# Kernel optimization log

Measured on AMD Instinct MI355X. Metric: run time of the kernel, lower is better.

## Reference

```python
import jax, jax.numpy as jnp
import numpy as np


def adder2d(x, w, stride=1, padding=0):
    """AdderNet conv: out = -sum_{ci,kh,kw} |x_patch - w|, supports groups.
    x: [B,Cin,H,W], w: [Cout, Cin//G, K, K]. Loops only over K*K kernel taps."""
    B, Cin, H, W = x.shape
    Cout, Cin_g, K, _ = w.shape
    G = Cin // Cin_g
    Co_g = Cout // G
    xp = jnp.pad(x, ((0, 0), (0, 0), (padding, padding), (padding, padding)))
    Ho = (H + 2 * padding - K) // stride + 1
    Wo = (W + 2 * padding - K) // stride + 1
    wg = w.reshape(G, Co_g, Cin_g, K, K)
    out = jnp.zeros((B, Cout, Ho, Wo), x.dtype)
    for kh in range(K):
        for kw in range(K):
            xs = jax.lax.slice(
                xp, (0, 0, kh, kw),
                (B, Cin, kh + stride * (Ho - 1) + 1, kw + stride * (Wo - 1) + 1),
                (1, 1, stride, stride))  # [B,Cin,Ho,Wo]
            xs = xs.reshape(B, G, 1, Cin_g, Ho, Wo)
            wt = wg[:, :, :, kh, kw][None, :, :, :, None, None]  # [1,G,Co_g,Cin_g,1,1]
            out = out - jnp.abs(xs - wt).sum(3).reshape(B, Cout, Ho, Wo)
    return out


def bn(x, g, b, m, v, eps=1e-5):
    inv = g / jnp.sqrt(v + eps)
    return x * inv[None, :, None, None] + (b - m * inv)[None, :, None, None]


def setup_inputs() -> dict:
    key = jax.random.key(0)
    ks = jax.random.split(key, 18)
    d = {}
    d["x"] = jax.random.normal(ks[0], (8, 256, 28, 28), jnp.float32)
    d["w1"] = jax.random.normal(ks[1], (64, 256, 1, 1), jnp.float32) * 0.05
    d["w_peg"] = jax.random.normal(ks[2], (64, 1, 3, 3), jnp.float32) * 0.05
    d["w2"] = jax.random.normal(ks[3], (64, 64, 3, 3), jnp.float32) * 0.05
    d["w3"] = jax.random.normal(ks[4], (256, 64, 1, 1), jnp.float32) * 0.05
    for i, (c, tag) in enumerate([(64, "1"), (64, "2"), (256, "3")]):
        d["g" + tag] = jax.random.uniform(ks[5 + 4 * i], (c,), jnp.float32, 0.5, 1.5)
        d["b" + tag] = jax.random.normal(ks[6 + 4 * i], (c,), jnp.float32) * 0.1
        d["m" + tag] = jax.random.normal(ks[7 + 4 * i], (c,), jnp.float32) * 0.1
        d["v" + tag] = jax.random.uniform(ks[8 + 4 * i], (c,), jnp.float32, 0.5, 1.5)
    return d


def reference(x, w1, w_peg, w2, w3, g1, b1, m1, v1, g2, b2, m2, v2, g3, b3, m3, v3):
    residual = x  # downsample is Identity (stride=1, inplanes==outplanes)
    h = adder2d(x, w1)                       # 1x1 adder conv 256->64
    h = adder2d(h, w_peg, stride=1, padding=1)  # PEG: depthwise 3x3 adder conv
    h = jax.nn.relu(bn(h, g1, b1, m1, v1))
    h = adder2d(h, w2, padding=1)            # 3x3 adder conv 64->64
    h = jax.nn.relu(bn(h, g2, b2, m2, v2))
    h = adder2d(h, w3)                       # 1x1 adder conv 64->256
    h = bn(h, g3, b3, m3, v3)
    return jax.nn.relu(h + residual)
```

## Files before the change

### kernel.cpp

```cpp
#include <hip/hip_runtime.h>
#include <math.h>

#define HW 28
#define PR 30
#define PC 32
#define PPAD (PR * PC)

__device__ __forceinline__ void tap3(const float4 a, const float2 b,
                                     const float w0, const float w1, const float w2,
                                     float4& acc) {
    acc.x += fabsf(a.x - w0) + fabsf(a.y - w1) + fabsf(a.z - w2);
    acc.y += fabsf(a.y - w0) + fabsf(a.z - w1) + fabsf(a.w - w2);
    acc.z += fabsf(a.z - w0) + fabsf(a.w - w1) + fabsf(b.x - w2);
    acc.w += fabsf(a.w - w0) + fabsf(b.x - w1) + fabsf(b.y - w2);
}

__global__ __launch_bounds__(448) void k1_adder1x1(const float* __restrict__ x,
                                                   const float* __restrict__ w1,
                                                   float* __restrict__ h1p) {
    __shared__ float  ws[256 * 20];
    __shared__ float4 pl[1792];
    const int tid    = threadIdx.x;
    const int cog    = tid & 3;
    const int pxg    = (tid >> 2) % 14;
    const int cic    = tid / 56;
    const int n      = blockIdx.x / 14;
    const int p0     = (blockIdx.x % 14) * 56 + pxg * 4;
    const int cobase = blockIdx.y * 16;

    for (int idx = tid; idx < 16 * 256; idx += 448) {
        int co = idx >> 8, ci = idx & 255;
        ws[ci * 20 + co] = w1[(size_t)(cobase + co) * 256 + ci];
    }
    __syncthreads();

    float4 acc0 = {0,0,0,0}, acc1 = acc0, acc2 = acc0, acc3 = acc0;
    const float* xp = x + ((size_t)n * 256 + cic * 32) * 784 + p0;
    const float* wp = ws + cic * 32 * 20 + cog * 4;
    #pragma unroll 4
    for (int i = 0; i < 32; ++i) {
        float4 u = *(const float4*)(xp + (size_t)i * 784);
        float4 w = *(const float4*)(wp + i * 20);
        acc0.x += fabsf(u.x - w.x); acc0.y += fabsf(u.y - w.x); acc0.z += fabsf(u.z - w.x); acc0.w += fabsf(u.w - w.x);
        acc1.x += fabsf(u.x - w.y); acc1.y += fabsf(u.y - w.y); acc1.z += fabsf(u.z - w.y); acc1.w += fabsf(u.w - w.y);
        acc2.x += fabsf(u.x - w.z); acc2.y += fabsf(u.y - w.z); acc2.z += fabsf(u.z - w.z); acc2.w += fabsf(u.w - w.z);
        acc3.x += fabsf(u.x - w.w); acc3.y += fabsf(u.y - w.w); acc3.z += fabsf(u.z - w.w); acc3.w += fabsf(u.w - w.w);
    }
    const int pbase = pxg * 16 + cog * 4;
    pl[cic * 224 + pbase + 0] = acc0;
    pl[cic * 224 + pbase + 1] = acc1;
    pl[cic * 224 + pbase + 2] = acc2;
    pl[cic * 224 + pbase + 3] = acc3;
    __syncthreads();

    if (tid < 224) {
        const int j = cic;
        float4 s = pl[pbase + j];
        #pragma unroll
        for (int c = 1; c < 8; ++c) {
            float4 t = pl[c * 224 + pbase + j];
            s.x += t.x; s.y += t.y; s.z += t.z; s.w += t.w;
        }
        const int co = cobase + cog * 4 + j;
        const int y = p0 / 28, xx = p0 % 28;
        float* op = h1p + ((size_t)(n * 64 + co) * PR + y + 1) * PC + xx + 1;
        op[0] = -s.x; op[1] = -s.y; op[2] = -s.z; op[3] = -s.w;
    }
}

__global__ __launch_bounds__(256) void k2_peg_bn_relu(const float* __restrict__ h1p,
                                                      const float* __restrict__ wp,
                                                      const float* __restrict__ g1,
                                                      const float* __restrict__ b1,
                                                      const float* __restrict__ m1,
                                                      const float* __restrict__ v1,
                                                      float* __restrict__ h2p) {
    const int t   = blockIdx.x * 256 + threadIdx.x;
    const int pxq = t % 196;
    const int c   = (t / 196) & 63;
    const int n   = t / (196 * 64);
    const int p0  = pxq * 4;
    const int y   = p0 / 28, xx = p0 % 28;

    const float* base = h1p + ((size_t)(n * 64 + c) * PR + y) * PC + xx;
    const float* wc   = wp + c * 9;
    float4 acc = {0,0,0,0};
    #pragma unroll
    for (int kh = 0; kh < 3; ++kh) {
        float4 a = *(const float4*)(base + kh * PC);
        float2 b = *(const float2*)(base + kh * PC + 4);
        tap3(a, b, wc[kh * 3 + 0], wc[kh * 3 + 1], wc[kh * 3 + 2], acc);
    }
    float inv = g1[c] * rsqrtf(v1[c] + 1e-5f);
    float bb  = b1[c] - m1[c] * inv;
    float* op = h2p + ((size_t)(n * 64 + c) * PR + y + 1) * PC + xx + 1;
    op[0] = fmaxf(-acc.x * inv + bb, 0.f);
    op[1] = fmaxf(-acc.y * inv + bb, 0.f);
    op[2] = fmaxf(-acc.z * inv + bb, 0.f);
    op[3] = fmaxf(-acc.w * inv + bb, 0.f);
}

__global__ __launch_bounds__(448) void k3_adder3x3_bn_relu(const float* __restrict__ h2p,
                                                           const float* __restrict__ w2,
                                                           const float* __restrict__ g2,
                                                           const float* __restrict__ b2,
                                                           const float* __restrict__ m2,
                                                           const float* __restrict__ v2,
                                                           float* __restrict__ h3) {
    __shared__ float  ws[576 * 20];
    __shared__ float4 pl[1792];
    const int tid    = threadIdx.x;
    const int cog    = tid & 3;
    const int pxg    = (tid >> 2) % 14;
    const int cic    = tid / 56;
    const int y0     = blockIdx.x * 2;
    const int cobase = blockIdx.y * 16;
    const int n      = blockIdx.z;
    const int yl     = pxg / 7;
    const int xx0    = (pxg % 7) * 4;
    const int Y      = y0 + yl;

    for (int idx = tid; idx < 9216; idx += 448) {
        int co = idx / 576;
        int rem = idx - co * 576;
        ws[rem * 20 + co] = w2[(size_t)(cobase + co) * 576 + rem];
    }
    __syncthreads();

    float4 acc0 = {0,0,0,0}, acc1 = acc0, acc2 = acc0, acc3 = acc0;
    #pragma unroll 2
    for (int i = 0; i < 8; ++i) {
        const float* rp = h2p + ((size_t)(n * 64 + cic * 8 + i) * PR + Y) * PC + xx0;
        const float* wb = ws + (cic * 8 + i) * 180 + cog * 4;
        #pragma unroll
        for (int kh = 0; kh < 3; ++kh) {
            float4 a = *(const float4*)(rp + kh * PC);
            float2 b = *(const float2*)(rp + kh * PC + 4);
            const float* wk = wb + kh * 60;
            float4 w0 = *(const float4*)(wk);
            float4 w1v = *(const float4*)(wk + 20);
            float4 w2v = *(const float4*)(wk + 40);
            tap3(a, b, w0.x, w1v.x, w2v.x, acc0);
            tap3(a, b, w0.y, w1v.y, w2v.y, acc1);
            tap3(a, b, w0.z, w1v.z, w2v.z, acc2);
            tap3(a, b, w0.w, w1v.w, w2v.w, acc3);
        }
    }
    const int pbase = pxg * 16 + cog * 4;
    pl[cic * 224 + pbase + 0] = acc0;
    pl[cic * 224 + pbase + 1] = acc1;
    pl[cic * 224 + pbase + 2] = acc2;
    pl[cic * 224 + pbase + 3] = acc3;
    __syncthreads();

    if (tid < 224) {
        const int j = cic;
        float4 s = pl[pbase + j];
        #pragma unroll
        for (int c = 1; c < 8; ++c) {
            float4 t = pl[c * 224 + pbase + j];
            s.x += t.x; s.y += t.y; s.z += t.z; s.w += t.w;
        }
        const int co = cobase + cog * 4 + j;
        float inv = g2[co] * rsqrtf(v2[co] + 1e-5f);
        float bb  = b2[co] - m2[co] * inv;
        float4 o;
        o.x = fmaxf(-s.x * inv + bb, 0.f);
        o.y = fmaxf(-s.y * inv + bb, 0.f);
        o.z = fmaxf(-s.z * inv + bb, 0.f);
        o.w = fmaxf(-s.w * inv + bb, 0.f);
        *(float4*)(h3 + (size_t)(n * 64 + co) * 784 + Y * 28 + xx0) = o;
    }
}

__global__ __launch_bounds__(448) void k6_adder1x1_bn_res_relu(const float* __restrict__ h3,
                                                               const float* __restrict__ w3,
                                                               const float* __restrict__ x,
                                                               const float* __restrict__ g3,
                                                               const float* __restrict__ b3,
                                                               const float* __restrict__ m3,
                                                               const float* __restrict__ v3,
                                                               float* __restrict__ out) {
    __shared__ float  ws[64 * 36];
    __shared__ float4 pl[1792];
    const int tid    = threadIdx.x;
    const int cog    = tid & 7;
    const int pxg    = (tid >> 3) % 14;
    const int cic    = tid / 112;
    const int n      = blockIdx.x / 14;
    const int p0     = (blockIdx.x % 14) * 56 + pxg * 4;
    const int cobase = blockIdx.y * 32;

    for (int idx = tid; idx < 2048; idx += 448) {
        int co = idx >> 6, ci = idx & 63;
        ws[ci * 36 + co] = w3[(size_t)(cobase + co) * 64 + ci];
    }
    __syncthreads();

    float4 acc0 = {0,0,0,0}, acc1 = acc0, acc2 = acc0, acc3 = acc0;
    const float* hp = h3 + ((size_t)n * 64 + cic * 16) * 784 + p0;
    const float* wp = ws + cic * 16 * 36 + cog * 4;
    #pragma unroll 4
    for (int i = 0; i < 16; ++i) {
        float4 u = *(const float4*)(hp + (size_t)i * 784);
        float4 w = *(const float4*)(wp + i * 36);
        acc0.x += fabsf(u.x - w.x); acc0.y += fabsf(u.y - w.x); acc0.z += fabsf(u.z - w.x); acc0.w += fabsf(u.w - w.x);
        acc1.x += fabsf(u.x - w.y); acc1.y += fabsf(u.y - w.y); acc1.z += fabsf(u.z - w.y); acc1.w += fabsf(u.w - w.y);
        acc2.x += fabsf(u.x - w.z); acc2.y += fabsf(u.y - w.z); acc2.z += fabsf(u.z - w.z); acc2.w += fabsf(u.w - w.z);
        acc3.x += fabsf(u.x - w.w); acc3.y += fabsf(u.y - w.w); acc3.z += fabsf(u.z - w.w); acc3.w += fabsf(u.w - w.w);
    }
    const int pbase = pxg * 32 + cog * 4;
    pl[cic * 448 + pbase + 0] = acc0;
    pl[cic * 448 + pbase + 1] = acc1;
    pl[cic * 448 + pbase + 2] = acc2;
    pl[cic * 448 + pbase + 3] = acc3;
    __syncthreads();

    {
        const int j = cic;
        float4 s = pl[pbase + j];
        #pragma unroll
        for (int c = 1; c < 4; ++c) {
            float4 t = pl[c * 448 + pbase + j];
            s.x += t.x; s.y += t.y; s.z += t.z; s.w += t.w;
        }
        const int co = cobase + cog * 4 + j;
        float inv = g3[co] * rsqrtf(v3[co] + 1e-5f);
        float bb  = b3[co] - m3[co] * inv;
        size_t obase = ((size_t)n * 256 + co) * 784 + p0;
        float4 r = *(const float4*)(x + obase);
        float4 o;
        o.x = fmaxf(-s.x * inv + bb + r.x, 0.f);
        o.y = fmaxf(-s.y * inv + bb + r.y, 0.f);
        o.z = fmaxf(-s.z * inv + bb + r.z, 0.f);
        o.w = fmaxf(-s.w * inv + bb + r.w, 0.f);
        *(float4*)(out + obase) = o;
    }
}

extern "C" void kernel_launch(void* const* d_in, const int* in_sizes, int n_in,
                              void* d_out, int out_size, void* d_ws, size_t ws_size,
                              hipStream_t stream) {
    const float* x  = (const float*)d_in[0];
    const float* w1 = (const float*)d_in[1];
    const float* wp = (const float*)d_in[2];
    const float* w2 = (const float*)d_in[3];
    const float* w3 = (const float*)d_in[4];
    const float* g1 = (const float*)d_in[5];
    const float* b1 = (const float*)d_in[6];
    const float* m1 = (const float*)d_in[7];
    const float* v1 = (const float*)d_in[8];
    const float* g2 = (const float*)d_in[9];
    const float* b2 = (const float*)d_in[10];
    const float* m2 = (const float*)d_in[11];
    const float* v2 = (const float*)d_in[12];
    const float* g3 = (const float*)d_in[13];
    const float* b3 = (const float*)d_in[14];
    const float* m3 = (const float*)d_in[15];
    const float* v3 = (const float*)d_in[16];
    float* out = (float*)d_out;

    float* h1p = (float*)d_ws;
    float* h2p = h1p + 491520;
    float* h3  = h2p + 491520;

    hipMemsetAsync(d_ws, 0, 2u * 491520u * 4u, stream);

    k1_adder1x1<<<dim3(112, 4), 448, 0, stream>>>(x, w1, h1p);
    k2_peg_bn_relu<<<dim3(392), 256, 0, stream>>>(h1p, wp, g1, b1, m1, v1, h2p);
    k3_adder3x3_bn_relu<<<dim3(14, 4, 8), 448, 0, stream>>>(h2p, w2, g2, b2, m2, v2, h3);
    k6_adder1x1_bn_res_relu<<<dim3(112, 8), 448, 0, stream>>>(h3, w3, x, g3, b3, m3, v3, out);
}
```

Measured before the change: 67.86 us.

## Fuse four adder-conv stages into two kernels with smem intermediates

Merges the 1x1 adder conv with the depthwise PEG conv and BN1, computing halo rows into shared memory per block. Merges the 3x3 adder conv, BN2, the final 1x1 adder conv, BN3 and the residual into one kernel per output row and image, keeping h3 in shared memory. Drops the h1 and h3 global buffers and the memset by writing the padding borders explicitly. In exchange it gives small grids (256 and 224 blocks), reloads the full w2/w3 weights per block, and recomputes halo rows in the first kernel.

```diff
diff --git a/kernel.cpp b/kernel.cpp
--- a/kernel.cpp
+++ b/kernel.cpp
@@ -1,10 +1,8 @@
 #include <hip/hip_runtime.h>
 #include <math.h>
 
-#define HW 28
 #define PR 30
 #define PC 32
-#define PPAD (PR * PC)
 
 __device__ __forceinline__ void tap3(const float4 a, const float2 b,
                                      const float w0, const float w1, const float w2,
@@ -15,226 +13,211 @@
     acc.w += fabsf(a.w - w0) + fabsf(b.x - w1) + fabsf(b.y - w2);
 }
 
-__global__ __launch_bounds__(448) void k1_adder1x1(const float* __restrict__ x,
-                                                   const float* __restrict__ w1,
-                                                   float* __restrict__ h1p) {
-    __shared__ float  ws[256 * 20];
-    __shared__ float4 pl[1792];
+__global__ __launch_bounds__(448) void ka_fused(const float* __restrict__ x,
+                                                const float* __restrict__ w1,
+                                                const float* __restrict__ wpeg,
+                                                const float* __restrict__ g1,
+                                                const float* __restrict__ b1,
+                                                const float* __restrict__ m1,
+                                                const float* __restrict__ v1,
+                                                float* __restrict__ h2p) {
+    __shared__ __align__(16) float smem[3072];
+    float* wsA = smem;
+    float* h1t = smem + 1024;
     const int tid    = threadIdx.x;
-    const int cog    = tid & 3;
-    const int pxg    = (tid >> 2) % 14;
-    const int cic    = tid / 56;
-    const int n      = blockIdx.x / 14;
-    const int p0     = (blockIdx.x % 14) * 56 + pxg * 4;
-    const int cobase = blockIdx.y * 16;
-
-    for (int idx = tid; idx < 16 * 256; idx += 448) {
-        int co = idx >> 8, ci = idx & 255;
-        ws[ci * 20 + co] = w1[(size_t)(cobase + co) * 256 + ci];
+    const int cobase = blockIdx.x * 4;
+    const int yh     = blockIdx.y;
+    const int n      = blockIdx.z;
+    const int co     = tid / 112;
+    const int rem    = tid % 112;
+    const int row    = rem / 7;
+    const int q      = rem % 7;
+
+    for (int idx = tid; idx < 1024; idx += 448) {
+        int c2 = idx >> 8, ci = idx & 255;
+        wsA[ci * 4 + c2] = w1[(size_t)(cobase + c2) * 256 + ci];
+    }
+    for (int idx = tid; idx < 512; idx += 448)
+        ((float4*)h1t)[idx] = make_float4(0.f, 0.f, 0.f, 0.f);
+    __syncthreads();
+
+    const int gy = yh * 14 - 1 + row;
+    if (gy >= 0 && gy < 28) {
+        float4 acc = {0.f, 0.f, 0.f, 0.f};
+        const float* xp = x + (size_t)n * 256 * 784 + gy * 28 + q * 4;
+        #pragma unroll 8
+        for (int ci = 0; ci < 256; ++ci) {
+            float4 u = *(const float4*)(xp + (size_t)ci * 784);
+            float w  = wsA[ci * 4 + co];
+            acc.x += fabsf(u.x - w); acc.y += fabsf(u.y - w);
+            acc.z += fabsf(u.z - w); acc.w += fabsf(u.w - w);
+        }
+        float* hd = h1t + co * 512 + row * 32 + 1 + q * 4;
+        hd[0] = -acc.x; hd[1] = -acc.y; hd[2] = -acc.z; hd[3] = -acc.w;
+    }
+    __syncthreads();
+
+    if (row < 14) {
+        const int c  = cobase + co;
+        const int oy = yh * 14 + row;
+        const float* wc = wpeg + c * 9;
+        const float* hb = h1t + co * 512 + row * 32 + q * 4;
+        float4 acc = {0.f, 0.f, 0.f, 0.f};
+        #pragma unroll
+        for (int kh = 0; kh < 3; ++kh) {
+            float4 a  = *(const float4*)(hb + kh * 32);
+            float2 bv = *(const float2*)(hb + kh * 32 + 4);
+            tap3(a, bv, wc[kh * 3 + 0], wc[kh * 3 + 1], wc[kh * 3 + 2], acc);
+        }
+        float inv = g1[c] * rsqrtf(v1[c] + 1e-5f);
+        float bb  = b1[c] - m1[c] * inv;
+        float* op = h2p + ((size_t)(n * 64 + c) * PR + oy + 1) * PC + 1 + q * 4;
+        op[0] = fmaxf(-acc.x * inv + bb, 0.f);
+        op[1] = fmaxf(-acc.y * inv + bb, 0.f);
+        op[2] = fmaxf(-acc.z * inv + bb, 0.f);
+        op[3] = fmaxf(-acc.w * inv + bb, 0.f);
+    }
+    for (int idx = tid; idx < 352; idx += 448) {
+        if (idx < 224) {
+            int rr = idx >> 4, k = idx & 15;
+            int cc = k >> 2, kk = k & 3;
+            int col = kk ? 28 + kk : 0;
+            h2p[((size_t)(n * 64 + cobase + cc) * PR + yh * 14 + 1 + rr) * PC + col] = 0.f;
+        } else {
+            int j = idx - 224;
+            int cc = j >> 5, col = j & 31;
+            int prow = yh ? 29 : 0;
+            h2p[((size_t)(n * 64 + cobase + cc) * PR + prow) * PC + col] = 0.f;
+        }
+    }
+}
+
+__global__ __launch_bounds__(448) void kb_fused(const float* __restrict__ h2p,
+                                                const float* __restrict__ w2,
+                                                const float* __restrict__ w3,
+                                                const float* __restrict__ x,
+                                                const float* __restrict__ g2,
+                                                const float* __restrict__ b2,
+                                                const float* __restrict__ m2,
+                                                const float* __restrict__ v2,
+                                                const float* __restrict__ g3,
+                                                const float* __restrict__ b3,
+                                                const float* __restrict__ m3,
+                                                const float* __restrict__ v3,
+                                                float* __restrict__ out) {
+    __shared__ __align__(16) float smem[18688];
+    float*  h3t = smem;
+    float*  h2t = smem + 2048;
+    float*  wck = smem + 8192;
+    float4* pl4 = (float4*)(smem + 2048);
+    float*  w3t = smem + 2048;
+    const int tid    = threadIdx.x;
+    const int Y      = blockIdx.x;
+    const int n      = blockIdx.y;
+    const int cic    = tid / 112;
+    const int rem    = tid % 112;
+    const int colane = rem / 7;
+    const int q      = rem % 7;
+
+    for (int idx = tid; idx < 1536; idx += 448) {
+        int ci = idx / 24, r2 = idx % 24;
+        int r = r2 / 8, c4 = r2 % 8;
+        *(float4*)(h2t + ci * 96 + r * 32 + c4 * 4) =
+            *(const float4*)(h2p + ((size_t)(n * 64 + ci) * PR + Y + r) * PC + c4 * 4);
     }
     __syncthreads();
 
     float4 acc0 = {0,0,0,0}, acc1 = acc0, acc2 = acc0, acc3 = acc0;
-    const float* xp = x + ((size_t)n * 256 + cic * 32) * 784 + p0;
-    const float* wp = ws + cic * 32 * 20 + cog * 4;
-    #pragma unroll 4
-    for (int i = 0; i < 32; ++i) {
-        float4 u = *(const float4*)(xp + (size_t)i * 784);
-        float4 w = *(const float4*)(wp + i * 20);
-        acc0.x += fabsf(u.x - w.x); acc0.y += fabsf(u.y - w.x); acc0.z += fabsf(u.z - w.x); acc0.w += fabsf(u.w - w.x);
-        acc1.x += fabsf(u.x - w.y); acc1.y += fabsf(u.y - w.y); acc1.z += fabsf(u.z - w.y); acc1.w += fabsf(u.w - w.y);
-        acc2.x += fabsf(u.x - w.z); acc2.y += fabsf(u.y - w.z); acc2.z += fabsf(u.z - w.z); acc2.w += fabsf(u.w - w.z);
-        acc3.x += fabsf(u.x - w.w); acc3.y += fabsf(u.y - w.w); acc3.z += fabsf(u.z - w.w); acc3.w += fabsf(u.w - w.w);
-    }
-    const int pbase = pxg * 16 + cog * 4;
-    pl[cic * 224 + pbase + 0] = acc0;
-    pl[cic * 224 + pbase + 1] = acc1;
-    pl[cic * 224 + pbase + 2] = acc2;
-    pl[cic * 224 + pbase + 3] = acc3;
-    __syncthreads();
-
-    if (tid < 224) {
-        const int j = cic;
-        float4 s = pl[pbase + j];
-        #pragma unroll
-        for (int c = 1; c < 8; ++c) {
-            float4 t = pl[c * 224 + pbase + j];
-            s.x += t.x; s.y += t.y; s.z += t.z; s.w += t.w;
-        }
-        const int co = cobase + cog * 4 + j;
-        const int y = p0 / 28, xx = p0 % 28;
-        float* op = h1p + ((size_t)(n * 64 + co) * PR + y + 1) * PC + xx + 1;
-        op[0] = -s.x; op[1] = -s.y; op[2] = -s.z; op[3] = -s.w;
-    }
-}
-
-__global__ __launch_bounds__(256) void k2_peg_bn_relu(const float* __restrict__ h1p,
-                                                      const float* __restrict__ wp,
-                                                      const float* __restrict__ g1,
-                                                      const float* __restrict__ b1,
-                                                      const float* __restrict__ m1,
-                                                      const float* __restrict__ v1,
-                                                      float* __restrict__ h2p) {
-    const int t   = blockIdx.x * 256 + threadIdx.x;
-    const int pxq = t % 196;
-    const int c   = (t / 196) & 63;
-    const int n   = t / (196 * 64);
-    const int p0  = pxq * 4;
-    const int y   = p0 / 28, xx = p0 % 28;
-
-    const float* base = h1p + ((size_t)(n * 64 + c) * PR + y) * PC + xx;
-    const float* wc   = wp + c * 9;
-    float4 acc = {0,0,0,0};
-    #pragma unroll
-    for (int kh = 0; kh < 3; ++kh) {
-        float4 a = *(const float4*)(base + kh * PC);
-        float2 b = *(const float2*)(base + kh * PC + 4);
-        tap3(a, b, wc[kh * 3 + 0], wc[kh * 3 + 1], wc[kh * 3 + 2], acc);
-    }
-    float inv = g1[c] * rsqrtf(v1[c] + 1e-5f);
-    float bb  = b1[c] - m1[c] * inv;
-    float* op = h2p + ((size_t)(n * 64 + c) * PR + y + 1) * PC + xx + 1;
-    op[0] = fmaxf(-acc.x * inv + bb, 0.f);
-    op[1] = fmaxf(-acc.y * inv + bb, 0.f);
-    op[2] = fmaxf(-acc.z * inv + bb, 0.f);
-    op[3] = fmaxf(-acc.w * inv + bb, 0.f);
-}
-
-__global__ __launch_bounds__(448) void k3_adder3x3_bn_relu(const float* __restrict__ h2p,
-                                                           const float* __restrict__ w2,
-                                                           const float* __restrict__ g2,
-                                                           const float* __restrict__ b2,
-                                                           const float* __restrict__ m2,
-                                                           const float* __restrict__ v2,
-                                                           float* __restrict__ h3) {
-    __shared__ float  ws[576 * 20];
-    __shared__ float4 pl[1792];
-    const int tid    = threadIdx.x;
-    const int cog    = tid & 3;
-    const int pxg    = (tid >> 2) % 14;
-    const int cic    = tid / 56;
-    const int y0     = blockIdx.x * 2;
-    const int cobase = blockIdx.y * 16;
-    const int n      = blockIdx.z;
-    const int yl     = pxg / 7;
-    const int xx0    = (pxg % 7) * 4;
-    const int Y      = y0 + yl;
-
-    for (int idx = tid; idx < 9216; idx += 448) {
-        int co = idx / 576;
-        int rem = idx - co * 576;
-        ws[rem * 20 + co] = w2[(size_t)(cobase + co) * 576 + rem];
-    }
-    __syncthreads();
-
-    float4 acc0 = {0,0,0,0}, acc1 = acc0, acc2 = acc0, acc3 = acc0;
-    #pragma unroll 2
-    for (int i = 0; i < 8; ++i) {
-        const float* rp = h2p + ((size_t)(n * 64 + cic * 8 + i) * PR + Y) * PC + xx0;
-        const float* wb = ws + (cic * 8 + i) * 180 + cog * 4;
-        #pragma unroll
-        for (int kh = 0; kh < 3; ++kh) {
-            float4 a = *(const float4*)(rp + kh * PC);
-            float2 b = *(const float2*)(rp + kh * PC + 4);
-            const float* wk = wb + kh * 60;
-            float4 w0 = *(const float4*)(wk);
-            float4 w1v = *(const float4*)(wk + 20);
-            float4 w2v = *(const float4*)(wk + 40);
-            tap3(a, b, w0.x, w1v.x, w2v.x, acc0);
-            tap3(a, b, w0.y, w1v.y, w2v.y, acc1);
-            tap3(a, b, w0.z, w1v.z, w2v.z, acc2);
-            tap3(a, b, w0.w, w1v.w, w2v.w, acc3);
-        }
-    }
-    const int pbase = pxg * 16 + cog * 4;
-    pl[cic * 224 + pbase + 0] = acc0;
-    pl[cic * 224 + pbase + 1] = acc1;
-    pl[cic * 224 + pbase + 2] = acc2;
-    pl[cic * 224 + pbase + 3] = acc3;
-    __syncthreads();
-
-    if (tid < 224) {
-        const int j = cic;
-        float4 s = pl[pbase + j];
-        #pragma unroll
-        for (int c = 1; c < 8; ++c) {
-            float4 t = pl[c * 224 + pbase + j];
-            s.x += t.x; s.y += t.y; s.z += t.z; s.w += t.w;
-        }
-        const int co = cobase + cog * 4 + j;
-        float inv = g2[co] * rsqrtf(v2[co] + 1e-5f);
-        float bb  = b2[co] - m2[co] * inv;
-        float4 o;
-        o.x = fmaxf(-s.x * inv + bb, 0.f);
-        o.y = fmaxf(-s.y * inv + bb, 0.f);
-        o.z = fmaxf(-s.z * inv + bb, 0.f);
-        o.w = fmaxf(-s.w * inv + bb, 0.f);
-        *(float4*)(h3 + (size_t)(n * 64 + co) * 784 + Y * 28 + xx0) = o;
-    }
-}
-
-__global__ __launch_bounds__(448) void k6_adder1x1_bn_res_relu(const float* __restrict__ h3,
-                                                               const float* __restrict__ w3,
-                                                               const float* __restrict__ x,
-                                                               const float* __restrict__ g3,
-                                                               const float* __restrict__ b3,
-                                                               const float* __restrict__ m3,
-                                                               const float* __restrict__ v3,
-                                                               float* __restrict__ out) {
-    __shared__ float  ws[64 * 36];
-    __shared__ float4 pl[1792];
-    const int tid    = threadIdx.x;
-    const int cog    = tid & 7;
-    const int pxg    = (tid >> 3) % 14;
-    const int cic    = tid / 112;
-    const int n      = blockIdx.x / 14;
-    const int p0     = (blockIdx.x % 14) * 56 + pxg * 4;
-    const int cobase = blockIdx.y * 32;
-
-    for (int idx = tid; idx < 2048; idx += 448) {
+    for (int ch = 0; ch < 4; ++ch) {
+        for (int idx = tid; idx < 9216; idx += 448) {
+            int co = idx / 144, r = idx % 144;
+            wck[r * 68 + co] = w2[(size_t)co * 576 + ch * 144 + r];
+        }
+        __syncthreads();
+        #pragma unroll
+        for (int i = 0; i < 4; ++i) {
+            const int cir = cic * 4 + i;
+            const int ci  = ch * 16 + cir;
+            const float* hb = h2t + ci * 96 + q * 4;
+            const float* wb = wck + cir * 612 + colane * 4;
+            #pragma unroll
+            for (int kh = 0; kh < 3; ++kh) {
+                float4 a  = *(const float4*)(hb + kh * 32);
+                float2 bv = *(const float2*)(hb + kh * 32 + 4);
+                float4 W0 = *(const float4*)(wb + (kh * 3 + 0) * 68);
+                float4 W1 = *(const float4*)(wb + (kh * 3 + 1) * 68);
+                float4 W2 = *(const float4*)(wb + (kh * 3 + 2) * 68);
+                tap3(a, bv, W0.x, W1.x, W2.x, acc0);
+                tap3(a, bv, W0.y, W1.y, W2.y, acc1);
+                tap3(a, bv, W0.z, W1.z, W2.z, acc2);
+                tap3(a, bv, W0.w, W1.w, W2.w, acc3);
+            }
+        }
+        __syncthreads();
+    }
+    pl4[tid * 4 + 0] = acc0;
+    pl4[tid * 4 + 1] = acc1;
+    pl4[tid * 4 + 2] = acc2;
+    pl4[tid * 4 + 3] = acc3;
+    __syncthreads();
+    if (tid < 112) {
+        #pragma unroll
+        for (int j = 0; j < 4; ++j) {
+            float4 s = pl4[tid * 4 + j];
+            #pragma unroll
+            for (int c = 1; c < 4; ++c) {
+                float4 t = pl4[(c * 112 + tid) * 4 + j];
+                s.x += t.x; s.y += t.y; s.z += t.z; s.w += t.w;
+            }
+            const int co = colane * 4 + j;
+            float inv = g2[co] * rsqrtf(v2[co] + 1e-5f);
+            float bb  = b2[co] - m2[co] * inv;
+            float4 o;
+            o.x = fmaxf(-s.x * inv + bb, 0.f);
+            o.y = fmaxf(-s.y * inv + bb, 0.f);
+            o.z = fmaxf(-s.z * inv + bb, 0.f);
+            o.w = fmaxf(-s.w * inv + bb, 0.f);
+            *(float4*)(h3t + co * 32 + q * 4) = o;
+        }
+    }
+    __syncthreads();
+
+    for (int idx = tid; idx < 16384; idx += 448) {
         int co = idx >> 6, ci = idx & 63;
-        ws[ci * 36 + co] = w3[(size_t)(cobase + co) * 64 + ci];
-    }
-    __syncthreads();
-
-    float4 acc0 = {0,0,0,0}, acc1 = acc0, acc2 = acc0, acc3 = acc0;
-    const float* hp = h3 + ((size_t)n * 64 + cic * 16) * 784 + p0;
-    const float* wp = ws + cic * 16 * 36 + cog * 4;
-    #pragma unroll 4
-    for (int i = 0; i < 16; ++i) {
-        float4 u = *(const float4*)(hp + (size_t)i * 784);
-        float4 w = *(const float4*)(wp + i * 36);
-        acc0.x += fabsf(u.x - w.x); acc0.y += fabsf(u.y - w.x); acc0.z += fabsf(u.z - w.x); acc0.w += fabsf(u.w - w.x);
-        acc1.x += fabsf(u.x - w.y); acc1.y += fabsf(u.y - w.y); acc1.z += fabsf(u.z - w.y); acc1.w += fabsf(u.w - w.y);
-        acc2.x += fabsf(u.x - w.z); acc2.y += fabsf(u.y - w.z); acc2.z += fabsf(u.z - w.z); acc2.w += fabsf(u.w - w.z);
-        acc3.x += fabsf(u.x - w.w); acc3.y += fabsf(u.y - w.w); acc3.z += fabsf(u.z - w.w); acc3.w += fabsf(u.w - w.w);
-    }
-    const int pbase = pxg * 32 + cog * 4;
-    pl[cic * 448 + pbase + 0] = acc0;
-    pl[cic * 448 + pbase + 1] = acc1;
-    pl[cic * 448 + pbase + 2] = acc2;
-    pl[cic * 448 + pbase + 3] = acc3;
+        w3t[ci * 260 + co] = w3[(size_t)co * 64 + ci];
+    }
     __syncthreads();
 
     {
-        const int j = cic;
-        float4 s = pl[pbase + j];
-        #pragma unroll
-        for (int c = 1; c < 4; ++c) {
-            float4 t = pl[c * 448 + pbase + j];
-            s.x += t.x; s.y += t.y; s.z += t.z; s.w += t.w;
-        }
-        const int co = cobase + cog * 4 + j;
-        float inv = g3[co] * rsqrtf(v3[co] + 1e-5f);
-        float bb  = b3[co] - m3[co] * inv;
-        size_t obase = ((size_t)n * 256 + co) * 784 + p0;
-        float4 r = *(const float4*)(x + obase);
-        float4 o;
-        o.x = fmaxf(-s.x * inv + bb + r.x, 0.f);
-        o.y = fmaxf(-s.y * inv + bb + r.y, 0.f);
-        o.z = fmaxf(-s.z * inv + bb + r.z, 0.f);
-        o.w = fmaxf(-s.w * inv + bb + r.w, 0.f);
-        *(float4*)(out + obase) = o;
+        const int bl = tid / 7;
+        const int bq = tid % 7;
+        float4 a0 = {0,0,0,0}, a1 = a0, a2 = a0, a3 = a0;
+        const float* hb = h3t + bq * 4;
+        const float* wb = w3t + bl * 4;
+        #pragma unroll 8
+        for (int ci = 0; ci < 64; ++ci) {
+            float4 h = *(const float4*)(hb + ci * 32);
+            float4 w = *(const float4*)(wb + ci * 260);
+            a0.x += fabsf(h.x - w.x); a0.y += fabsf(h.y - w.x); a0.z += fabsf(h.z - w.x); a0.w += fabsf(h.w - w.x);
+            a1.x += fabsf(h.x - w.y); a1.y += fabsf(h.y - w.y); a1.z += fabsf(h.z - w.y); a1.w += fabsf(h.w - w.y);
+            a2.x += fabsf(h.x - w.z); a2.y += fabsf(h.y - w.z); a2.z += fabsf(h.z - w.z); a2.w += fabsf(h.w - w.z);
+            a3.x += fabsf(h.x - w.w); a3.y += fabsf(h.y - w.w); a3.z += fabsf(h.z - w.w); a3.w += fabsf(h.w - w.w);
+        }
+        float4 accs[4] = {a0, a1, a2, a3};
+        #pragma unroll
+        for (int j = 0; j < 4; ++j) {
+            const int co = bl * 4 + j;
+            float inv = g3[co] * rsqrtf(v3[co] + 1e-5f);
+            float bb  = b3[co] - m3[co] * inv;
+            size_t obase = ((size_t)n * 256 + co) * 784 + Y * 28 + bq * 4;
+            float4 r = *(const float4*)(x + obase);
+            float4 o;
+            o.x = fmaxf(-accs[j].x * inv + bb + r.x, 0.f);
+            o.y = fmaxf(-accs[j].y * inv + bb + r.y, 0.f);
+            o.z = fmaxf(-accs[j].z * inv + bb + r.z, 0.f);
+            o.w = fmaxf(-accs[j].w * inv + bb + r.w, 0.f);
+            *(float4*)(out + obase) = o;
+        }
     }
 }
 
@@ -260,14 +243,9 @@
     const float* v3 = (const float*)d_in[16];
     float* out = (float*)d_out;
 
-    float* h1p = (float*)d_ws;
-    float* h2p = h1p + 491520;
-    float* h3  = h2p + 491520;
-
-    hipMemsetAsync(d_ws, 0, 2u * 491520u * 4u, stream);
-
-    k1_adder1x1<<<dim3(112, 4), 448, 0, stream>>>(x, w1, h1p);
-    k2_peg_bn_relu<<<dim3(392), 256, 0, stream>>>(h1p, wp, g1, b1, m1, v1, h2p);
-    k3_adder3x3_bn_relu<<<dim3(14, 4, 8), 448, 0, stream>>>(h2p, w2, g2, b2, m2, v2, h3);
-    k6_adder1x1_bn_res_relu<<<dim3(112, 8), 448, 0, stream>>>(h3, w3, x, g3, b3, m3, v3, out);
-}
+    float* h2p = (float*)d_ws;
+
+    ka_fused<<<dim3(16, 2, 8), 448, 0, stream>>>(x, w1, wp, g1, b1, m1, v1, h2p);
+    kb_fused<<<dim3(28, 8), 448, 0, stream>>>(h2p, w2, w3, x,
+                                              g2, b2, m2, v2, g3, b3, m3, v3, out);
+}
```

Result: slower. 73.48 us (+8.3%).
